# Kernel optimization log

Hardware: AMD Instinct MI355X
Metric: run time of the kernel (lower is better)

## Reference

```python
import jax, jax.numpy as jnp
import numpy as np

D_MODEL = 1024
D_FF = 4096
NUM_EXPERTS = 8
TOP_K = 2


def setup_inputs() -> dict:
    key = jax.random.key(0)
    ks = jax.random.split(key, 10)
    s = 0.02
    x = jax.random.normal(ks[0], (2, 1024, D_MODEL), dtype=jnp.float32)
    # router gate (nn.Linear(d_model, num_experts))
    Wr = jax.random.normal(ks[1], (D_MODEL, NUM_EXPERTS), dtype=jnp.float32) * s
    br = jnp.zeros((NUM_EXPERTS,), dtype=jnp.float32)
    # stacked expert weights
    Wg = jax.random.normal(ks[2], (NUM_EXPERTS, D_MODEL, D_FF), dtype=jnp.float32) * s
    bg = jnp.zeros((NUM_EXPERTS, D_FF), dtype=jnp.float32)
    Wu = jax.random.normal(ks[3], (NUM_EXPERTS, D_MODEL, D_FF), dtype=jnp.float32) * s
    bu = jnp.zeros((NUM_EXPERTS, D_FF), dtype=jnp.float32)
    Wd = jax.random.normal(ks[4], (NUM_EXPERTS, D_FF, D_MODEL), dtype=jnp.float32) * s
    bd = jnp.zeros((NUM_EXPERTS, D_MODEL), dtype=jnp.float32)
    return {"x": x, "Wr": Wr, "br": br, "Wg": Wg, "bg": bg,
            "Wu": Wu, "bu": bu, "Wd": Wd, "bd": bd}


def reference(x, Wr, br, Wg, bg, Wu, bu, Wd, bd):
    B, S, D = x.shape
    E = Wg.shape[0]
    xt = x.reshape(-1, D)                       # [T, d]
    T = xt.shape[0]
    # router: softmax in float32, top-k, renormalize (Mixtral-style)
    logits = xt @ Wr + br                       # [T, E]
    probs = jax.nn.softmax(logits.astype(jnp.float32), axis=-1)
    rw, sel = jax.lax.top_k(probs, TOP_K)       # [T, K]
    rw = rw / jnp.sum(rw, axis=-1, keepdims=True)
    # per-token per-expert combine weight (0 if expert not selected)
    w_full = jnp.zeros((T, E), dtype=rw.dtype).at[
        jnp.arange(T)[:, None], sel].add(rw)    # [T, E]
    # SwiGLU experts, computed densely over all tokens then masked-combined
    g = jnp.einsum('td,edf->etf', xt, Wg) + bg[:, None, :]   # [E, T, f]
    u = jnp.einsum('td,edf->etf', xt, Wu) + bu[:, None, :]
    h = jax.nn.silu(g) * u
    y = jnp.einsum('etf,efd->etd', h, Wd) + bd[:, None, :]    # [E, T, d]
    out = jnp.einsum('te,etd->td', w_full.astype(x.dtype), y)
    return out.reshape(B, S, D)
```

## Files before the change

### kernel.cpp

```cpp
#include <hip/hip_runtime.h>

typedef float floatx4 __attribute__((ext_vector_type(4)));
typedef __bf16 bf16x2 __attribute__((ext_vector_type(2)));
typedef __bf16 bf16x4 __attribute__((ext_vector_type(4)));
typedef __bf16 bf16x8 __attribute__((ext_vector_type(8)));

#define D_MODEL 1024
#define D_FF 4096
#define NE 8

__device__ __forceinline__ void gload16(const void* g, void* l) {
    __builtin_amdgcn_global_load_lds(
        (const __attribute__((address_space(1))) void*)g,
        (__attribute__((address_space(3))) void*)l, 16, 0, 0);
}

__device__ __forceinline__ int frag_off(int row, int q) {
    return row * 32 + ((q ^ ((row >> 2) & 3)) << 3);
}

__device__ __forceinline__ unsigned int pk(float lo, float hi) {
    union { bf16x2 v; unsigned int u; } c;
    c.v = bf16x2{(__bf16)lo, (__bf16)hi};
    return c.u;
}

__global__ __launch_bounds__(256) void router_kernel(
    const float* __restrict__ x, const float* __restrict__ Wr,
    const float* __restrict__ br, int* __restrict__ cnt,
    int* __restrict__ list, float* __restrict__ w_slot, int T)
{
    int wv = threadIdx.x >> 6;
    int lane = threadIdx.x & 63;
    int t = blockIdx.x * 4 + wv;
    if (t >= T) return;

    const float* xp = x + (size_t)t * D_MODEL;
    float acc[8] = {0.f,0.f,0.f,0.f,0.f,0.f,0.f,0.f};
#pragma unroll
    for (int i = 0; i < 16; ++i) {
        int d = i * 64 + lane;
        float xv = xp[d];
        float4 w0 = *(const float4*)(Wr + d * 8);
        float4 w1 = *(const float4*)(Wr + d * 8 + 4);
        acc[0] += xv * w0.x; acc[1] += xv * w0.y;
        acc[2] += xv * w0.z; acc[3] += xv * w0.w;
        acc[4] += xv * w1.x; acc[5] += xv * w1.y;
        acc[6] += xv * w1.z; acc[7] += xv * w1.w;
    }
#pragma unroll
    for (int off = 32; off >= 1; off >>= 1) {
#pragma unroll
        for (int e = 0; e < 8; ++e)
            acc[e] += __shfl_down(acc[e], off, 64);
    }
    if (lane == 0) {
        float l[8];
#pragma unroll
        for (int e = 0; e < 8; ++e) l[e] = acc[e] + br[e];
        int i0 = 0; float v0 = l[0];
#pragma unroll
        for (int e = 1; e < 8; ++e) if (l[e] > v0) { v0 = l[e]; i0 = e; }
        int i1 = -1; float v1 = -3.4e38f;
#pragma unroll
        for (int e = 0; e < 8; ++e) if (e != i0 && l[e] > v1) { v1 = l[e]; i1 = e; }
        float ex = __expf(v1 - v0);
        float w0 = 1.f / (1.f + ex);
        float w1 = ex / (1.f + ex);
        int p0 = atomicAdd(&cnt[i0], 1);
        list[i0 * T + p0] = 2 * t;
        int p1 = atomicAdd(&cnt[i1], 1);
        list[i1 * T + p1] = 2 * t + 1;
        w_slot[2 * t]     = w0;
        w_slot[2 * t + 1] = w1;
    }
}

__global__ __launch_bounds__(256) void prep_kernel(
    const float* __restrict__ Wg, const float* __restrict__ Wu,
    const float* __restrict__ Wd, const float* __restrict__ x,
    __bf16* __restrict__ Wgt, __bf16* __restrict__ Wut,
    __bf16* __restrict__ Wdt, __bf16* __restrict__ Xb)
{
    const int bid = blockIdx.x;
    const int tid = threadIdx.x;
    if (bid >= 24576) {
        int base = (bid - 24576) * 2048 + tid * 8;
        float4 v0 = *(const float4*)(x + base);
        float4 v1 = *(const float4*)(x + base + 4);
        bf16x8 o = {(__bf16)v0.x, (__bf16)v0.y, (__bf16)v0.z, (__bf16)v0.w,
                    (__bf16)v1.x, (__bf16)v1.y, (__bf16)v1.z, (__bf16)v1.w};
        *(bf16x8*)(Xb + base) = o;
        return;
    }
    const int tensor = bid >> 13;
    const int rem = bid & 8191;
    const int e = rem >> 10;
    const int tile = rem & 1023;
    const float* src; __bf16* dst; int K, N, kb, nb;
    if (tensor == 0)      { src = Wg; dst = Wgt; }
    else if (tensor == 1) { src = Wu; dst = Wut; }
    else                  { src = Wd; dst = Wdt; }
    if (tensor < 2) { K = 1024; N = 4096; kb = (tile & 15) << 6; nb = (tile >> 4) << 6; }
    else            { K = 4096; N = 1024; kb = (tile & 63) << 6; nb = (tile >> 6) << 6; }
    src += (size_t)e * K * N + (size_t)kb * N + nb;
    dst += (size_t)e * K * N + (size_t)nb * K + kb;

    __shared__ unsigned int tp[64 * 33];

    const int p  = tid >> 3;
    const int ci = tid & 7;
    const float* s0 = src + (size_t)(2 * p) * N + 4 * ci;
    float4 r0a = *(const float4*)(s0);
    float4 r0b = *(const float4*)(s0 + 32);
    float4 r1a = *(const float4*)(s0 + N);
    float4 r1b = *(const float4*)(s0 + N + 32);

    unsigned int* w0 = &tp[(4 * ci) * 33 + p];
    w0[0]  = pk(r0a.x, r1a.x);
    w0[33] = pk(r0a.y, r1a.y);
    w0[66] = pk(r0a.z, r1a.z);
    w0[99] = pk(r0a.w, r1a.w);
    unsigned int* w1 = &tp[(4 * ci + 32) * 33 + p];
    w1[0]  = pk(r0b.x, r1b.x);
    w1[33] = pk(r0b.y, r1b.y);
    w1[66] = pk(r0b.z, r1b.z);
    w1[99] = pk(r0b.w, r1b.w);
    __syncthreads();

    const int r = tid >> 2;
    const int q = tid & 3;
    const unsigned int* rp = &tp[r * 33 + q * 8];
    uint4 oa = {rp[0], rp[1], rp[2], rp[3]};
    uint4 ob = {rp[4], rp[5], rp[6], rp[7]};
    __bf16* drow = dst + (size_t)r * K + q * 16;
    *(uint4*)(drow)     = oa;
    *(uint4*)(drow + 8) = ob;
}

__global__ __launch_bounds__(256, 3) void gateup3_kernel(
    const __bf16* __restrict__ Xb, const __bf16* __restrict__ Wgt,
    const __bf16* __restrict__ Wut, const float* __restrict__ bg,
    const float* __restrict__ bu, const int* __restrict__ cnt,
    const int* __restrict__ list, __bf16* __restrict__ H, int T)
{
    const int e  = blockIdx.z;
    const int m0 = blockIdx.y * 128;
    const int n0 = blockIdx.x * 64;
    const int count = cnt[e];
    if (m0 >= count) return;

    __shared__ __bf16 ldsA[4096];
    __shared__ __bf16 ldsBg[2048];
    __shared__ __bf16 ldsBu[2048];
    __shared__ int s_entry[128];

    const int tid = threadIdx.x;
    if (tid < 128) {
        int r = m0 + tid;
        s_entry[tid] = (r < count) ? list[e * T + r] : list[e * T];
    }
    __syncthreads();

    const int row0 = tid >> 2, j0 = tid & 3;
    const int g0 = j0 ^ ((row0 >> 2) & 3);
    const int p1 = 256 + tid, row1 = p1 >> 2, j1 = p1 & 3;
    const int g1 = j1 ^ ((row1 >> 2) & 3);
    const __bf16* asrc0 = Xb + (size_t)(s_entry[row0] >> 1) * D_MODEL + g0 * 8;
    const __bf16* asrc1 = Xb + (size_t)(s_entry[row1] >> 1) * D_MODEL + g1 * 8;
    const __bf16* gsrc  = Wgt + ((size_t)e * D_FF + n0 + row0) * D_MODEL + g0 * 8;
    const __bf16* usrc  = Wut + ((size_t)e * D_FF + n0 + row0) * D_MODEL + g0 * 8;
    char* adst0 = (char*)ldsA + tid * 16;
    char* adst1 = (char*)ldsA + (256 + tid) * 16;
    char* gdst  = (char*)ldsBg + tid * 16;
    char* udst  = (char*)ldsBu + tid * 16;

    const int wv = tid >> 6, lane = tid & 63;
    const int wm = wv >> 1, wn = wv & 1;
    const int q = lane >> 4, ln = lane & 15;
    int aoff[4], boff[2];
#pragma unroll
    for (int i = 0; i < 4; ++i) aoff[i] = frag_off(wm * 64 + i * 16 + ln, q);
#pragma unroll
    for (int i = 0; i < 2; ++i) boff[i] = frag_off(wn * 32 + i * 16 + ln, q);

    floatx4 accg[4][2] = {};
    floatx4 accu[4][2] = {};

    for (int k0 = 0; k0 < D_MODEL; k0 += 32) {
        gload16(asrc0 + k0, adst0);
        gload16(asrc1 + k0, adst1);
        gload16(gsrc + k0, gdst);
        gload16(usrc + k0, udst);
        __syncthreads();

        bf16x8 af[4], bgf[2], buf[2];
#pragma unroll
        for (int i = 0; i < 4; ++i) af[i]  = *(const bf16x8*)&ldsA[aoff[i]];
#pragma unroll
        for (int i = 0; i < 2; ++i) bgf[i] = *(const bf16x8*)&ldsBg[boff[i]];
#pragma unroll
        for (int i = 0; i < 2; ++i) buf[i] = *(const bf16x8*)&ldsBu[boff[i]];
#pragma unroll
        for (int mi = 0; mi < 4; ++mi)
#pragma unroll
            for (int ni = 0; ni < 2; ++ni) {
                accg[mi][ni] = __builtin_amdgcn_mfma_f32_16x16x32_bf16(af[mi], bgf[ni], accg[mi][ni], 0, 0, 0);
                accu[mi][ni] = __builtin_amdgcn_mfma_f32_16x16x32_bf16(af[mi], buf[ni], accu[mi][ni], 0, 0, 0);
            }
        __syncthreads();
    }

#pragma unroll
    for (int ni = 0; ni < 2; ++ni) {
        int col = n0 + wn * 32 + ni * 16 + ln;
        float bgv = bg[e * D_FF + col];
        float buv = bu[e * D_FF + col];
#pragma unroll
        for (int mi = 0; mi < 4; ++mi) {
            int lrow0 = wm * 64 + mi * 16 + q * 4;
#pragma unroll
            for (int r = 0; r < 4; ++r) {
                int lr = lrow0 + r;
                if (m0 + lr < count) {
                    int entry = s_entry[lr];
                    float g = accg[mi][ni][r] + bgv;
                    float u = accu[mi][ni][r] + buv;
                    float h = g / (1.f + __expf(-g)) * u;
                    H[(size_t)entry * D_FF + col] = (__bf16)h;
                }
            }
        }
    }
}

__global__ __launch_bounds__(256, 3) void down3_kernel(
    const __bf16* __restrict__ H, const __bf16* __restrict__ Wdt,
    const float* __restrict__ bd, const int* __restrict__ cnt,
    const int* __restrict__ list, float* __restrict__ Y, int T)
{
    const int e  = blockIdx.z >> 1;
    const int kc = blockIdx.z & 1;
    const int m0 = blockIdx.y * 128;
    const int n0 = blockIdx.x * 128;
    const int count = cnt[e];
    if (m0 >= count) return;

    __shared__ __bf16 ldsA[4096];
    __shared__ __bf16 ldsB[4096];
    __shared__ int s_entry[128];

    const int tid = threadIdx.x;
    if (tid < 128) {
        int r = m0 + tid;
        s_entry[tid] = (r < count) ? list[e * T + r] : list[e * T];
    }
    __syncthreads();

    const int kbase = kc * (D_FF / 2);
    const __bf16* asrc[2]; const __bf16* bsrc[2];
    char* adst[2]; char* bdst[2];
#pragma unroll
    for (int i = 0; i < 2; ++i) {
        int p = i * 256 + tid;
        int row = p >> 2, j = p & 3;
        int g = j ^ ((row >> 2) & 3);
        asrc[i] = H + (size_t)s_entry[row] * D_FF + kbase + g * 8;
        bsrc[i] = Wdt + ((size_t)e * D_MODEL + n0 + row) * D_FF + kbase + g * 8;
        adst[i] = (char*)ldsA + (size_t)p * 16;
        bdst[i] = (char*)ldsB + (size_t)p * 16;
    }

    const int wv = tid >> 6, lane = tid & 63;
    const int wm = wv >> 1, wn = wv & 1;
    const int q = lane >> 4, ln = lane & 15;
    int aoff[4], boff[4];
#pragma unroll
    for (int i = 0; i < 4; ++i) {
        aoff[i] = frag_off(wm * 64 + i * 16 + ln, q);
        boff[i] = frag_off(wn * 64 + i * 16 + ln, q);
    }

    floatx4 acc[4][4] = {};

    for (int k0 = 0; k0 < D_FF / 2; k0 += 32) {
#pragma unroll
        for (int i = 0; i < 2; ++i) {
            gload16(asrc[i] + k0, adst[i]);
            gload16(bsrc[i] + k0, bdst[i]);
        }
        __syncthreads();

        bf16x8 af[4], bf[4];
#pragma unroll
        for (int i = 0; i < 4; ++i) af[i] = *(const bf16x8*)&ldsA[aoff[i]];
#pragma unroll
        for (int i = 0; i < 4; ++i) bf[i] = *(const bf16x8*)&ldsB[boff[i]];
#pragma unroll
        for (int mi = 0; mi < 4; ++mi)
#pragma unroll
            for (int ni = 0; ni < 4; ++ni)
                acc[mi][ni] = __builtin_amdgcn_mfma_f32_16x16x32_bf16(af[mi], bf[ni], acc[mi][ni], 0, 0, 0);
        __syncthreads();
    }

    const size_t kc_off = (size_t)kc * 2 * T * D_MODEL;
#pragma unroll
    for (int ni = 0; ni < 4; ++ni) {
        int col = n0 + wn * 64 + ni * 16 + ln;
        float bdv = (kc == 0) ? bd[e * D_MODEL + col] : 0.f;
#pragma unroll
        for (int mi = 0; mi < 4; ++mi) {
            int lrow0 = wm * 64 + mi * 16 + q * 4;
#pragma unroll
            for (int r = 0; r < 4; ++r) {
                int lr = lrow0 + r;
                if (m0 + lr < count) {
                    int entry = s_entry[lr];
                    Y[kc_off + (size_t)entry * D_MODEL + col] = acc[mi][ni][r] + bdv;
                }
            }
        }
    }
}

__global__ __launch_bounds__(256) void combine_kernel(
    const float* __restrict__ Y, const float* __restrict__ w_slot,
    float* __restrict__ out, int T)
{
    int idx = blockIdx.x * 256 + threadIdx.x;
    int t = idx >> 8;
    const float4* Y4 = (const float4*)Y;
    size_t r0 = (size_t)(2 * t) * 256 + (idx & 255);
    size_t r1 = r0 + 256;
    size_t ks = (size_t)2 * T * 256;
    float4 a = Y4[r0], b = Y4[r1];
#pragma unroll
    for (int kc = 1; kc < 2; ++kc) {
        float4 va = Y4[r0 + kc * ks], vb = Y4[r1 + kc * ks];
        a.x += va.x; a.y += va.y; a.z += va.z; a.w += va.w;
        b.x += vb.x; b.y += vb.y; b.z += vb.z; b.w += vb.w;
    }
    float w0 = w_slot[2 * t], w1 = w_slot[2 * t + 1];
    float4 o = {w0 * a.x + w1 * b.x, w0 * a.y + w1 * b.y,
                w0 * a.z + w1 * b.z, w0 * a.w + w1 * b.w};
    ((float4*)out)[idx] = o;
}

extern "C" void kernel_launch(void* const* d_in, const int* in_sizes, int n_in,
                              void* d_out, int out_size, void* d_ws, size_t ws_size,
                              hipStream_t stream) {
    const float* x  = (const float*)d_in[0];
    const float* Wr = (const float*)d_in[1];
    const float* br = (const float*)d_in[2];
    const float* Wg = (const float*)d_in[3];
    const float* bg = (const float*)d_in[4];
    const float* Wu = (const float*)d_in[5];
    const float* bu = (const float*)d_in[6];
    const float* Wd = (const float*)d_in[7];
    const float* bd = (const float*)d_in[8];
    float* out = (float*)d_out;
    const int T = in_sizes[0] / D_MODEL;

    char* ws = (char*)d_ws;
    size_t off = 256;
    int*   cnt    = (int*)ws;
    int*   list   = (int*)(ws + off);              off += (size_t)NE * T * 4;
    float* w_slot = (float*)(ws + off);            off += (size_t)2 * T * 4;
    off = (off + 1023) & ~(size_t)1023;
    __bf16* Xb  = (__bf16*)(ws + off);             off += (size_t)T * D_MODEL * 2;
    __bf16* H   = (__bf16*)(ws + off);             off += (size_t)2 * T * D_FF * 2;
    __bf16* Wgt = (__bf16*)(ws + off);
    float*  Y   = (float*)(ws + off);
    off += (size_t)NE * D_MODEL * D_FF * 2;
    __bf16* Wut = (__bf16*)(ws + off);             off += (size_t)NE * D_MODEL * D_FF * 2;
    __bf16* Wdt = (__bf16*)(ws + off);             off += (size_t)NE * D_FF * D_MODEL * 2;

    hipMemsetAsync(cnt, 0, 256, stream);

    router_kernel<<<dim3((T + 3) / 4), dim3(256), 0, stream>>>(x, Wr, br, cnt, list, w_slot, T);

    prep_kernel<<<dim3(25600), dim3(256), 0, stream>>>(Wg, Wu, Wd, x, Wgt, Wut, Wdt, Xb);

    dim3 gb(D_FF / 64, (T + 127) / 128, NE);
    gateup3_kernel<<<gb, dim3(256), 0, stream>>>(Xb, Wgt, Wut, bg, bu, cnt, list, H, T);

    dim3 gc(D_MODEL / 128, (T + 127) / 128, NE * 2);
    down3_kernel<<<gc, dim3(256), 0, stream>>>(H, Wdt, bd, cnt, list, Y, T);

    combine_kernel<<<dim3(T * D_MODEL / 4 / 256), dim3(256), 0, stream>>>(Y, w_slot, out, T);
}
```

Baseline: 675.0 us.

## Double GEMM K-step to 64 and raise down-projection split-K to four

Both expert GEMM kernels now stage 64-wide K slices in LDS per iteration, split into two 32-wide sub-slices, which halves the number of barrier-separated load rounds. The down-projection also splits K four ways instead of two, giving more blocks for parallelism. The combine kernel sums four partial Y buffers, which doubles partial-sum memory traffic. LDS use per block also doubles, which may reduce occupancy.

After: 677.2 us. No clear change (+0.3%).

```diff
diff --git a/kernel.cpp b/kernel.cpp
--- a/kernel.cpp
+++ b/kernel.cpp
@@ -150,9 +150,9 @@
     const int count = cnt[e];
     if (m0 >= count) return;
 
-    __shared__ __bf16 ldsA[4096];
-    __shared__ __bf16 ldsBg[2048];
-    __shared__ __bf16 ldsBu[2048];
+    __shared__ __bf16 ldsA[8192];
+    __shared__ __bf16 ldsBg[4096];
+    __shared__ __bf16 ldsBu[4096];
     __shared__ int s_entry[128];
 
     const int tid = threadIdx.x;
@@ -162,18 +162,28 @@
     }
     __syncthreads();
 
-    const int row0 = tid >> 2, j0 = tid & 3;
-    const int g0 = j0 ^ ((row0 >> 2) & 3);
-    const int p1 = 256 + tid, row1 = p1 >> 2, j1 = p1 & 3;
-    const int g1 = j1 ^ ((row1 >> 2) & 3);
-    const __bf16* asrc0 = Xb + (size_t)(s_entry[row0] >> 1) * D_MODEL + g0 * 8;
-    const __bf16* asrc1 = Xb + (size_t)(s_entry[row1] >> 1) * D_MODEL + g1 * 8;
-    const __bf16* gsrc  = Wgt + ((size_t)e * D_FF + n0 + row0) * D_MODEL + g0 * 8;
-    const __bf16* usrc  = Wut + ((size_t)e * D_FF + n0 + row0) * D_MODEL + g0 * 8;
-    char* adst0 = (char*)ldsA + tid * 16;
-    char* adst1 = (char*)ldsA + (256 + tid) * 16;
-    char* gdst  = (char*)ldsBg + tid * 16;
-    char* udst  = (char*)ldsBu + tid * 16;
+    const __bf16* asrc[4]; char* adst[4];
+#pragma unroll
+    for (int i = 0; i < 4; ++i) {
+        int p = i * 256 + tid;
+        int s = p >> 9;
+        int row = (p & 511) >> 2, j = p & 3;
+        int g = j ^ ((row >> 2) & 3);
+        asrc[i] = Xb + (size_t)(s_entry[row] >> 1) * D_MODEL + s * 32 + g * 8;
+        adst[i] = (char*)ldsA + p * 16;
+    }
+    const __bf16* gsrc[2]; const __bf16* usrc[2]; char* gdst[2]; char* udst[2];
+#pragma unroll
+    for (int i = 0; i < 2; ++i) {
+        int p = i * 256 + tid;
+        int s = p >> 8;
+        int row = (p & 255) >> 2, j = p & 3;
+        int g = j ^ ((row >> 2) & 3);
+        gsrc[i] = Wgt + ((size_t)e * D_FF + n0 + row) * D_MODEL + s * 32 + g * 8;
+        usrc[i] = Wut + ((size_t)e * D_FF + n0 + row) * D_MODEL + s * 32 + g * 8;
+        gdst[i] = (char*)ldsBg + p * 16;
+        udst[i] = (char*)ldsBu + p * 16;
+    }
 
     const int wv = tid >> 6, lane = tid & 63;
     const int wm = wv >> 1, wn = wv & 1;
@@ -187,27 +197,33 @@
     floatx4 accg[4][2] = {};
     floatx4 accu[4][2] = {};
 
-    for (int k0 = 0; k0 < D_MODEL; k0 += 32) {
-        gload16(asrc0 + k0, adst0);
-        gload16(asrc1 + k0, adst1);
-        gload16(gsrc + k0, gdst);
-        gload16(usrc + k0, udst);
+    for (int k0 = 0; k0 < D_MODEL; k0 += 64) {
+#pragma unroll
+        for (int i = 0; i < 4; ++i) gload16(asrc[i] + k0, adst[i]);
+#pragma unroll
+        for (int i = 0; i < 2; ++i) {
+            gload16(gsrc[i] + k0, gdst[i]);
+            gload16(usrc[i] + k0, udst[i]);
+        }
         __syncthreads();
 
-        bf16x8 af[4], bgf[2], buf[2];
-#pragma unroll
-        for (int i = 0; i < 4; ++i) af[i]  = *(const bf16x8*)&ldsA[aoff[i]];
-#pragma unroll
-        for (int i = 0; i < 2; ++i) bgf[i] = *(const bf16x8*)&ldsBg[boff[i]];
-#pragma unroll
-        for (int i = 0; i < 2; ++i) buf[i] = *(const bf16x8*)&ldsBu[boff[i]];
-#pragma unroll
-        for (int mi = 0; mi < 4; ++mi)
-#pragma unroll
-            for (int ni = 0; ni < 2; ++ni) {
-                accg[mi][ni] = __builtin_amdgcn_mfma_f32_16x16x32_bf16(af[mi], bgf[ni], accg[mi][ni], 0, 0, 0);
-                accu[mi][ni] = __builtin_amdgcn_mfma_f32_16x16x32_bf16(af[mi], buf[ni], accu[mi][ni], 0, 0, 0);
-            }
+#pragma unroll
+        for (int s = 0; s < 2; ++s) {
+            bf16x8 af[4], bgf[2], buf[2];
+#pragma unroll
+            for (int i = 0; i < 4; ++i) af[i]  = *(const bf16x8*)&ldsA[s * 4096 + aoff[i]];
+#pragma unroll
+            for (int i = 0; i < 2; ++i) bgf[i] = *(const bf16x8*)&ldsBg[s * 2048 + boff[i]];
+#pragma unroll
+            for (int i = 0; i < 2; ++i) buf[i] = *(const bf16x8*)&ldsBu[s * 2048 + boff[i]];
+#pragma unroll
+            for (int mi = 0; mi < 4; ++mi)
+#pragma unroll
+                for (int ni = 0; ni < 2; ++ni) {
+                    accg[mi][ni] = __builtin_amdgcn_mfma_f32_16x16x32_bf16(af[mi], bgf[ni], accg[mi][ni], 0, 0, 0);
+                    accu[mi][ni] = __builtin_amdgcn_mfma_f32_16x16x32_bf16(af[mi], buf[ni], accu[mi][ni], 0, 0, 0);
+                }
+        }
         __syncthreads();
     }
 
@@ -239,15 +255,15 @@
     const float* __restrict__ bd, const int* __restrict__ cnt,
     const int* __restrict__ list, float* __restrict__ Y, int T)
 {
-    const int e  = blockIdx.z >> 1;
-    const int kc = blockIdx.z & 1;
+    const int e  = blockIdx.z >> 2;
+    const int kc = blockIdx.z & 3;
     const int m0 = blockIdx.y * 128;
     const int n0 = blockIdx.x * 128;
     const int count = cnt[e];
     if (m0 >= count) return;
 
-    __shared__ __bf16 ldsA[4096];
-    __shared__ __bf16 ldsB[4096];
+    __shared__ __bf16 ldsA[8192];
+    __shared__ __bf16 ldsB[8192];
     __shared__ int s_entry[128];
 
     const int tid = threadIdx.x;
@@ -257,18 +273,19 @@
     }
     __syncthreads();
 
-    const int kbase = kc * (D_FF / 2);
-    const __bf16* asrc[2]; const __bf16* bsrc[2];
-    char* adst[2]; char* bdst[2];
-#pragma unroll
-    for (int i = 0; i < 2; ++i) {
+    const int kbase = kc * (D_FF / 4);
+    const __bf16* asrc[4]; const __bf16* bsrc[4];
+    char* adst[4]; char* bdst[4];
+#pragma unroll
+    for (int i = 0; i < 4; ++i) {
         int p = i * 256 + tid;
-        int row = p >> 2, j = p & 3;
+        int s = p >> 9;
+        int row = (p & 511) >> 2, j = p & 3;
         int g = j ^ ((row >> 2) & 3);
-        asrc[i] = H + (size_t)s_entry[row] * D_FF + kbase + g * 8;
-        bsrc[i] = Wdt + ((size_t)e * D_MODEL + n0 + row) * D_FF + kbase + g * 8;
-        adst[i] = (char*)ldsA + (size_t)p * 16;
-        bdst[i] = (char*)ldsB + (size_t)p * 16;
+        asrc[i] = H + (size_t)s_entry[row] * D_FF + kbase + s * 32 + g * 8;
+        bsrc[i] = Wdt + ((size_t)e * D_MODEL + n0 + row) * D_FF + kbase + s * 32 + g * 8;
+        adst[i] = (char*)ldsA + p * 16;
+        bdst[i] = (char*)ldsB + p * 16;
     }
 
     const int wv = tid >> 6, lane = tid & 63;
@@ -283,24 +300,27 @@
 
     floatx4 acc[4][4] = {};
 
-    for (int k0 = 0; k0 < D_FF / 2; k0 += 32) {
-#pragma unroll
-        for (int i = 0; i < 2; ++i) {
+    for (int k0 = 0; k0 < D_FF / 4; k0 += 64) {
+#pragma unroll
+        for (int i = 0; i < 4; ++i) {
             gload16(asrc[i] + k0, adst[i]);
             gload16(bsrc[i] + k0, bdst[i]);
         }
         __syncthreads();
 
-        bf16x8 af[4], bf[4];
-#pragma unroll
-        for (int i = 0; i < 4; ++i) af[i] = *(const bf16x8*)&ldsA[aoff[i]];
-#pragma unroll
-        for (int i = 0; i < 4; ++i) bf[i] = *(const bf16x8*)&ldsB[boff[i]];
-#pragma unroll
-        for (int mi = 0; mi < 4; ++mi)
-#pragma unroll
-            for (int ni = 0; ni < 4; ++ni)
-                acc[mi][ni] = __builtin_amdgcn_mfma_f32_16x16x32_bf16(af[mi], bf[ni], acc[mi][ni], 0, 0, 0);
+#pragma unroll
+        for (int s = 0; s < 2; ++s) {
+            bf16x8 af[4], bf[4];
+#pragma unroll
+            for (int i = 0; i < 4; ++i) af[i] = *(const bf16x8*)&ldsA[s * 4096 + aoff[i]];
+#pragma unroll
+            for (int i = 0; i < 4; ++i) bf[i] = *(const bf16x8*)&ldsB[s * 4096 + boff[i]];
+#pragma unroll
+            for (int mi = 0; mi < 4; ++mi)
+#pragma unroll
+                for (int ni = 0; ni < 4; ++ni)
+                    acc[mi][ni] = __builtin_amdgcn_mfma_f32_16x16x32_bf16(af[mi], bf[ni], acc[mi][ni], 0, 0, 0);
+        }
         __syncthreads();
     }
 
@@ -336,7 +356,7 @@
     size_t ks = (size_t)2 * T * 256;
     float4 a = Y4[r0], b = Y4[r1];
 #pragma unroll
-    for (int kc = 1; kc < 2; ++kc) {
+    for (int kc = 1; kc < 4; ++kc) {
         float4 va = Y4[r0 + kc * ks], vb = Y4[r1 + kc * ks];
         a.x += va.x; a.y += va.y; a.z += va.z; a.w += va.w;
         b.x += vb.x; b.y += vb.y; b.z += vb.z; b.w += vb.w;
@@ -385,7 +405,7 @@
     dim3 gb(D_FF / 64, (T + 127) / 128, NE);
     gateup3_kernel<<<gb, dim3(256), 0, stream>>>(Xb, Wgt, Wut, bg, bu, cnt, list, H, T);
 
-    dim3 gc(D_MODEL / 128, (T + 127) / 128, NE * 2);
+    dim3 gc(D_MODEL / 128, (T + 127) / 128, NE * 4);
     down3_kernel<<<gc, dim3(256), 0, stream>>>(H, Wdt, bd, cnt, list, Y, T);
 
     combine_kernel<<<dim3(T * D_MODEL / 4 / 256), dim3(256), 0, stream>>>(Y, w_slot, out, T);
```
